# Kernel optimization log

Measured on AMD Instinct MI355X. Metric: run time of the kernel, lower is better.

Reference implementation:

```python
import jax, jax.numpy as jnp
import numpy as np

B, N, E, H = 32, 512, 256, 8
HD = E // H
EPS = 1e-5

def setup_inputs() -> dict:
    key = jax.random.key(0)
    ks = jax.random.split(key, 10)
    x = jax.random.normal(ks[0], (B, N, E), dtype=jnp.float32)
    # boolean masks: True = masked out. Keep diagonal unmasked so no row is fully masked.
    pre = jax.random.bernoulli(ks[1], 0.1, (B, H, N, N))
    eye = jnp.eye(N, dtype=bool)
    pre_mask = jnp.where(eye[None, None, :, :], False, pre)
    post_attn_mask = jax.random.bernoulli(ks[2], 0.1, (B, N))
    s = 1.0 / np.sqrt(E)
    in_proj_w = jax.random.uniform(ks[3], (3 * E, E), jnp.float32, -s, s)
    in_proj_b = jnp.zeros((3 * E,), jnp.float32)
    out_w = jax.random.uniform(ks[4], (E, E), jnp.float32, -s, s)
    out_b = jnp.zeros((E,), jnp.float32)
    gamma = jnp.ones((E,), jnp.float32)
    beta = jnp.zeros((E,), jnp.float32)
    return {"x": x, "pre_mask": pre_mask, "post_attn_mask": post_attn_mask,
            "in_proj_w": in_proj_w, "in_proj_b": in_proj_b,
            "out_w": out_w, "out_b": out_b, "gamma": gamma, "beta": beta}

def reference(x, pre_mask, post_attn_mask, in_proj_w, in_proj_b, out_w, out_b, gamma, beta):
    b, n, e = x.shape
    # fused qkv projection (matches nn.MultiheadAttention in_proj)
    qkv = x @ in_proj_w.T + in_proj_b            # [B,N,3E]
    q, k, v = jnp.split(qkv, 3, axis=-1)
    def heads(t):
        return t.reshape(b, n, H, HD).transpose(0, 2, 1, 3)  # [B,H,N,HD]
    q, k, v = heads(q), heads(k), heads(v)
    scores = jnp.einsum('bhqd,bhkd->bhqk', q * (HD ** -0.5), k)  # [B,H,N,N]
    scores = jnp.where(pre_mask, -1e9, scores)
    w = jax.nn.softmax(scores, axis=-1)                          # [B,H,N,N]
    o = jnp.einsum('bhqk,bhkd->bhqd', w, v)                      # [B,H,N,HD]
    o = o.transpose(0, 2, 1, 3).reshape(b, n, e)
    o = o @ out_w.T + out_b
    # post-attention mask: zero outputs of unavailable agents
    o = jnp.where(post_attn_mask[:, :, None], 0.0, o)
    # residual + LayerNorm
    y = x + o
    mu = y.mean(axis=-1, keepdims=True)
    var = y.var(axis=-1, keepdims=True)
    out = (y - mu) * jax.lax.rsqrt(var + EPS) * gamma + beta
    # attn_weights averaged over heads (PyTorch default average_attn_weights=True)
    attn_weights = w.mean(axis=1)                                # [B,N,N]
    return (out, attn_weights)
```

## Files before the change

### kernel.cpp

```cpp
#include <hip/hip_runtime.h>

#define BB 32
#define NN 512
#define EE 256
#define HH 8
#define HDD 32

typedef __attribute__((ext_vector_type(4))) float f32x4;
typedef __attribute__((ext_vector_type(8))) short s16x8;
typedef unsigned short ushort_t;
typedef unsigned int uint_t;

__device__ __forceinline__ ushort_t f2bf(float f) {
  union { float f; uint_t u; } v; v.f = f;
  uint_t r = v.u + 0x7fffu + ((v.u >> 16) & 1u);
  return (ushort_t)(r >> 16);
}
__device__ __forceinline__ uint_t pk2(float a, float b) {
  return (uint_t)f2bf(a) | ((uint_t)f2bf(b) << 16);
}
__device__ __forceinline__ float bf2f(ushort_t u) {
  union { uint_t u; float f; } v; v.u = ((uint_t)u) << 16;
  return v.f;
}

__global__ __launch_bounds__(256) void cvt_all(
    const float* __restrict__ x, const float* __restrict__ w1, const float* __restrict__ w2,
    ushort_t* __restrict__ xb, ushort_t* __restrict__ w1b, ushort_t* __restrict__ w2b) {
  const int NX = BB * NN * EE / 4;
  const int NW1 = 3 * EE * EE / 4;
  const int NW2 = EE * EE / 4;
  int i = blockIdx.x * 256 + threadIdx.x;
  const float* src; ushort_t* dst; int j;
  if (i < NX) { src = x; dst = xb; j = i; }
  else if (i < NX + NW1) { src = w1; dst = w1b; j = i - NX; }
  else if (i < NX + NW1 + NW2) { src = w2; dst = w2b; j = i - NX - NW1; }
  else return;
  float4 v = ((const float4*)src)[j];
  uint2 p; p.x = pk2(v.x, v.y); p.y = pk2(v.z, v.w);
  ((uint2*)dst)[j] = p;
}

__global__ __launch_bounds__(256) void qkv_mfma(
    const ushort_t* __restrict__ xb, const ushort_t* __restrict__ wb,
    const float* __restrict__ bias,
    ushort_t* __restrict__ Q, ushort_t* __restrict__ K, ushort_t* __restrict__ Vt) {
  __shared__ ushort_t sA[128][40];
  __shared__ ushort_t sB[128][40];
  int t = threadIdx.x;
  int bj = blockIdx.x % 6, bm = blockIdx.x / 6;
  int m0 = bm * 128, j0 = bj * 128;
  int w4 = t >> 6, lane = t & 63, quad = lane >> 4, l16 = lane & 15;
  int wy = w4 >> 1, wx = w4 & 1;
  f32x4 acc[4][4];
  #pragma unroll
  for (int a = 0; a < 4; a++)
    #pragma unroll
    for (int b = 0; b < 4; b++) acc[a][b] = (f32x4){0.f, 0.f, 0.f, 0.f};
  int sr2 = t >> 2, sc2 = (t & 3) * 8;
  for (int kk = 0; kk < 256; kk += 32) {
    __syncthreads();
    #pragma unroll
    for (int p = 0; p < 2; p++) {
      int r = sr2 + 64 * p;
      *(s16x8*)&sA[r][sc2] = *(const s16x8*)&xb[(size_t)(m0 + r) * 256 + kk + sc2];
      *(s16x8*)&sB[r][sc2] = *(const s16x8*)&wb[(size_t)(j0 + r) * 256 + kk + sc2];
    }
    __syncthreads();
    s16x8 af[4], bf[4];
    #pragma unroll
    for (int mt = 0; mt < 4; mt++)
      af[mt] = *(const s16x8*)&sA[wy * 64 + mt * 16 + l16][quad * 8];
    #pragma unroll
    for (int jt = 0; jt < 4; jt++)
      bf[jt] = *(const s16x8*)&sB[wx * 64 + jt * 16 + l16][quad * 8];
    #pragma unroll
    for (int mt = 0; mt < 4; mt++)
      #pragma unroll
      for (int jt = 0; jt < 4; jt++)
        acc[mt][jt] = __builtin_amdgcn_mfma_f32_16x16x32_bf16(af[mt], bf[jt], acc[mt][jt], 0, 0, 0);
  }
  #pragma unroll
  for (int jt = 0; jt < 4; jt++) {
    int j = j0 + wx * 64 + jt * 16 + l16;
    int which = j >> 8, e0 = j & 255, h = e0 >> 5, d0 = e0 & 31;
    float b = bias[j];
    #pragma unroll
    for (int mt = 0; mt < 4; mt++) {
      #pragma unroll
      for (int r = 0; r < 4; r++) {
        int m = m0 + wy * 64 + mt * 16 + quad * 4 + r;
        int bi = m >> 9, n = m & 511;
        ushort_t val = f2bf(acc[mt][jt][r] + b);
        if (which == 2) {
          Vt[((size_t)(bi * 8 + h) * 32 + d0) * 512 + n] = val;
        } else {
          ushort_t* dst = (which == 0) ? Q : K;
          dst[((size_t)(bi * 8 + h) * 512 + n) * 32 + d0] = val;
        }
      }
    }
  }
}

__global__ __launch_bounds__(256, 4) void attn_fused(
    const ushort_t* __restrict__ Q, const ushort_t* __restrict__ K,
    const ushort_t* __restrict__ Vt, const int* __restrict__ pre_mask,
    const ushort_t* __restrict__ wob, const float* __restrict__ x,
    const float* __restrict__ out_b, const int* __restrict__ post_mask,
    const float* __restrict__ gamma, const float* __restrict__ beta,
    float* __restrict__ out, float* __restrict__ attnw) {
  __shared__ ushort_t sP[4][16 * 132];
  __shared__ float sSum[2][4][16];
  __shared__ float sO[4][16 * 33];
  __shared__ ushort_t sO16[16 * 260];
  __shared__ float sRed1[16][4];
  __shared__ float sRed2[16][4];

  int t = threadIdx.x;
  int bb = blockIdx.x >> 5;
  int q0 = (blockIdx.x & 31) << 4;
  int w = t >> 6, lane = t & 63, quad = lane >> 4, l16 = lane & 15;
  int kbase = w * 128;
  const float scale = 0.17677669529663687f;
  ushort_t* mysP = &sP[w][0];

  uint_t wm[16];
  #pragma unroll
  for (int i = 0; i < 16; i++) wm[i] = 0u;

  for (int h = 0; h < 8; h++) {
    size_t base = ((size_t)(bb * 8 + h) * 512) * 32;
    const int* mbase = pre_mask + ((size_t)(bb * 8 + h) * 512 + q0) * 512;

    int mreg[32];
    #pragma unroll
    for (int t8 = 0; t8 < 8; t8++)
      #pragma unroll
      for (int i = 0; i < 4; i++)
        mreg[t8 * 4 + i] = mbase[(quad * 4 + i) * 512 + kbase + t8 * 16 + l16];

    s16x8 afrag = *(const s16x8*)&Q[base + (size_t)(q0 + l16) * 32 + quad * 8];

    float psum[4] = {0.f, 0.f, 0.f, 0.f};
    #pragma unroll
    for (int t8 = 0; t8 < 8; t8++) {
      int n0 = kbase + t8 * 16;
      s16x8 bfrag = *(const s16x8*)&K[base + (size_t)(n0 + l16) * 32 + quad * 8];
      f32x4 acc = {0.f, 0.f, 0.f, 0.f};
      acc = __builtin_amdgcn_mfma_f32_16x16x32_bf16(afrag, bfrag, acc, 0, 0, 0);
      #pragma unroll
      for (int i = 0; i < 4; i++) {
        float e = mreg[t8 * 4 + i] ? 0.f : __expf(acc[i] * scale);
        mysP[(quad * 4 + i) * 132 + t8 * 16 + l16] = f2bf(e);
        psum[i] += e;
      }
    }
    #pragma unroll
    for (int i = 0; i < 4; i++) {
      float s = psum[i];
      s += __shfl_xor(s, 1, 64);
      s += __shfl_xor(s, 2, 64);
      s += __shfl_xor(s, 4, 64);
      s += __shfl_xor(s, 8, 64);
      psum[i] = s;
    }
    if (l16 == 0) {
      #pragma unroll
      for (int i = 0; i < 4; i++) sSum[h & 1][w][quad * 4 + i] = psum[i];
    }
    __syncthreads();

    float inv[4];
    #pragma unroll
    for (int i = 0; i < 4; i++) {
      int r = quad * 4 + i;
      inv[i] = 0.125f / (sSum[h & 1][0][r] + sSum[h & 1][1][r] + sSum[h & 1][2][r] + sSum[h & 1][3][r]);
    }
    #pragma unroll
    for (int i = 0; i < 4; i++) {
      #pragma unroll
      for (int t4 = 0; t4 < 4; t4++) {
        float a0 = inv[i] * bf2f(mysP[(quad * 4 + i) * 132 + (2 * t4) * 16 + l16]);
        float a1 = inv[i] * bf2f(mysP[(quad * 4 + i) * 132 + (2 * t4 + 1) * 16 + l16]);
        uint_t cur = wm[i * 4 + t4];
        wm[i * 4 + t4] = pk2(bf2f((ushort_t)(cur & 0xffffu)) + a0,
                             bf2f((ushort_t)(cur >> 16)) + a1);
      }
    }

    f32x4 oacc[2];
    oacc[0] = (f32x4){0.f, 0.f, 0.f, 0.f};
    oacc[1] = (f32x4){0.f, 0.f, 0.f, 0.f};
    #pragma unroll
    for (int ks = 0; ks < 4; ks++) {
      s16x8 pa = *(const s16x8*)&mysP[l16 * 132 + ks * 32 + quad * 8];
      #pragma unroll
      for (int dt = 0; dt < 2; dt++) {
        s16x8 vb = *(const s16x8*)&Vt[base + (size_t)(dt * 16 + l16) * 512 + kbase + ks * 32 + quad * 8];
        oacc[dt] = __builtin_amdgcn_mfma_f32_16x16x32_bf16(pa, vb, oacc[dt], 0, 0, 0);
      }
    }
    #pragma unroll
    for (int dt = 0; dt < 2; dt++)
      #pragma unroll
      for (int i = 0; i < 4; i++)
        sO[w][(quad * 4 + i) * 33 + dt * 16 + l16] = oacc[dt][i];
    __syncthreads();

    {
      int r = t >> 4;
      int c = (t & 15) * 2;
      float s0 = sO[0][r * 33 + c] + sO[1][r * 33 + c] + sO[2][r * 33 + c] + sO[3][r * 33 + c];
      float s1 = sO[0][r * 33 + c + 1] + sO[1][r * 33 + c + 1] + sO[2][r * 33 + c + 1] + sO[3][r * 33 + c + 1];
      float invr = 1.0f / (sSum[h & 1][0][r] + sSum[h & 1][1][r] + sSum[h & 1][2][r] + sSum[h & 1][3][r]);
      *(uint_t*)&sO16[r * 260 + h * 32 + c] = pk2(s0 * invr, s1 * invr);
    }
  }

  {
    float* arow = attnw + (size_t)(bb * 512 + q0) * 512;
    #pragma unroll
    for (int i = 0; i < 4; i++) {
      #pragma unroll
      for (int t4 = 0; t4 < 4; t4++) {
        uint_t c = wm[i * 4 + t4];
        arow[(quad * 4 + i) * 512 + kbase + (2 * t4) * 16 + l16] = bf2f((ushort_t)(c & 0xffffu));
        arow[(quad * 4 + i) * 512 + kbase + (2 * t4 + 1) * 16 + l16] = bf2f((ushort_t)(c >> 16));
      }
    }
  }
  __syncthreads();

  int jr0 = w * 64;
  f32x4 pacc[4];
  #pragma unroll
  for (int jt = 0; jt < 4; jt++) pacc[jt] = (f32x4){0.f, 0.f, 0.f, 0.f};
  #pragma unroll
  for (int kc = 0; kc < 8; kc++) {
    s16x8 pa = *(const s16x8*)&sO16[l16 * 260 + kc * 32 + quad * 8];
    #pragma unroll
    for (int jt = 0; jt < 4; jt++) {
      s16x8 bf = *(const s16x8*)&wob[(size_t)(jr0 + jt * 16 + l16) * 256 + kc * 32 + quad * 8];
      pacc[jt] = __builtin_amdgcn_mfma_f32_16x16x32_bf16(pa, bf, pacc[jt], 0, 0, 0);
    }
  }

  float g4[4], bt4[4], ob4[4];
  #pragma unroll
  for (int jt = 0; jt < 4; jt++) {
    int j = jr0 + jt * 16 + l16;
    g4[jt] = gamma[j]; bt4[jt] = beta[j]; ob4[jt] = out_b[j];
  }
  float yv[4][4];
  #pragma unroll
  for (int i = 0; i < 4; i++) {
    int r = quad * 4 + i;
    int m = bb * 512 + q0 + r;
    bool msk = post_mask[m] != 0;
    float s1 = 0.f, s2 = 0.f;
    #pragma unroll
    for (int jt = 0; jt < 4; jt++) {
      int j = jr0 + jt * 16 + l16;
      float p = msk ? 0.f : (pacc[jt][i] + ob4[jt]);
      float yy = x[(size_t)m * 256 + j] + p;
      yv[i][jt] = yy; s1 += yy; s2 += yy * yy;
    }
    s1 += __shfl_xor(s1, 1, 64); s1 += __shfl_xor(s1, 2, 64);
    s1 += __shfl_xor(s1, 4, 64); s1 += __shfl_xor(s1, 8, 64);
    s2 += __shfl_xor(s2, 1, 64); s2 += __shfl_xor(s2, 2, 64);
    s2 += __shfl_xor(s2, 4, 64); s2 += __shfl_xor(s2, 8, 64);
    if (l16 == 0) { sRed1[r][w] = s1; sRed2[r][w] = s2; }
  }
  __syncthreads();
  #pragma unroll
  for (int i = 0; i < 4; i++) {
    int r = quad * 4 + i;
    int m = bb * 512 + q0 + r;
    float S1 = sRed1[r][0] + sRed1[r][1] + sRed1[r][2] + sRed1[r][3];
    float S2 = sRed2[r][0] + sRed2[r][1] + sRed2[r][2] + sRed2[r][3];
    float mu = S1 * (1.0f / 256.0f);
    float var = S2 * (1.0f / 256.0f) - mu * mu;
    float rstd = rsqrtf(var + 1e-5f);
    #pragma unroll
    for (int jt = 0; jt < 4; jt++) {
      int j = jr0 + jt * 16 + l16;
      out[(size_t)m * 256 + j] = (yv[i][jt] - mu) * rstd * g4[jt] + bt4[jt];
    }
  }
}

extern "C" void kernel_launch(void* const* d_in, const int* in_sizes, int n_in,
                              void* d_out, int out_size, void* d_ws, size_t ws_size,
                              hipStream_t stream) {
  const float* x       = (const float*)d_in[0];
  const int*   pre_m   = (const int*)d_in[1];
  const int*   post_m  = (const int*)d_in[2];
  const float* in_w    = (const float*)d_in[3];
  const float* in_b    = (const float*)d_in[4];
  const float* out_w   = (const float*)d_in[5];
  const float* out_b   = (const float*)d_in[6];
  const float* gamma   = (const float*)d_in[7];
  const float* beta    = (const float*)d_in[8];
  float* out   = (float*)d_out;
  float* attnw = out + (size_t)BB * NN * EE;
  ushort_t* Q   = (ushort_t*)d_ws;
  ushort_t* K   = Q  + (size_t)BB * HH * NN * HDD;
  ushort_t* Vt  = K  + (size_t)BB * HH * NN * HDD;
  ushort_t* xb  = Vt + (size_t)BB * HH * NN * HDD;
  ushort_t* wib = xb + (size_t)BB * NN * EE;
  ushort_t* wob = wib + (size_t)3 * EE * EE;

  const int NCVT = BB * NN * EE / 4 + 3 * EE * EE / 4 + EE * EE / 4;
  cvt_all<<<dim3((NCVT + 255) / 256), dim3(256), 0, stream>>>(x, in_w, out_w, xb, wib, wob);
  qkv_mfma<<<dim3(768), dim3(256), 0, stream>>>(xb, wib, in_b, Q, K, Vt);
  attn_fused<<<dim3(1024), dim3(256), 0, stream>>>(Q, K, Vt, pre_m, wob, x, out_b, post_m,
                                                   gamma, beta, out, attnw);
}
```

Measured before the change: 461.5 us.

## Pack the attention mask to bits alongside the QKV GEMM and read bits in attention

Extra blocks are added to the QKV projection launch. They convert the int32 pre-attention mask into a packed bitmask in workspace while the GEMM blocks run. The attention kernel then loads four uint4 bit-rows per head instead of 32 strided int32 loads, and extracts each mask bit with a shift. This aims to hide the large mask read behind the compute-bound GEMM and to cut memory latency inside the attention loop. The cost is an extra bitmask write and read in workspace, plus GEMM blocks sharing the device with bandwidth-heavy compression blocks.

```diff
diff --git a/kernel.cpp b/kernel.cpp
--- a/kernel.cpp
+++ b/kernel.cpp
@@ -41,13 +41,36 @@
   ((uint2*)dst)[j] = p;
 }
 
-__global__ __launch_bounds__(256) void qkv_mfma(
+#define NQKV 768
+#define NCMP 1280
+__global__ __launch_bounds__(256) void qkv_compress(
     const ushort_t* __restrict__ xb, const ushort_t* __restrict__ wb,
     const float* __restrict__ bias,
-    ushort_t* __restrict__ Q, ushort_t* __restrict__ K, ushort_t* __restrict__ Vt) {
+    ushort_t* __restrict__ Q, ushort_t* __restrict__ K, ushort_t* __restrict__ Vt,
+    const int* __restrict__ pre_mask, uint_t* __restrict__ mbits) {
   __shared__ ushort_t sA[128][40];
   __shared__ ushort_t sB[128][40];
   int t = threadIdx.x;
+
+  if (blockIdx.x >= NQKV) {
+    const int NWRD = BB * HH * NN * NN / 32;
+    const int STR = NCMP * 256;
+    for (int wi = (blockIdx.x - NQKV) * 256 + t; wi < NWRD; wi += STR) {
+      const int4* p = (const int4*)pre_mask + (size_t)wi * 8;
+      uint_t bits = 0u;
+      #pragma unroll
+      for (int j = 0; j < 8; j++) {
+        int4 v = p[j];
+        bits |= (uint_t)(v.x != 0) << (j * 4);
+        bits |= (uint_t)(v.y != 0) << (j * 4 + 1);
+        bits |= (uint_t)(v.z != 0) << (j * 4 + 2);
+        bits |= (uint_t)(v.w != 0) << (j * 4 + 3);
+      }
+      mbits[wi] = bits;
+    }
+    return;
+  }
+
   int bj = blockIdx.x % 6, bm = blockIdx.x / 6;
   int m0 = bm * 128, j0 = bj * 128;
   int w4 = t >> 6, lane = t & 63, quad = lane >> 4, l16 = lane & 15;
@@ -105,7 +128,7 @@
 
 __global__ __launch_bounds__(256, 4) void attn_fused(
     const ushort_t* __restrict__ Q, const ushort_t* __restrict__ K,
-    const ushort_t* __restrict__ Vt, const int* __restrict__ pre_mask,
+    const ushort_t* __restrict__ Vt, const uint_t* __restrict__ mbits32,
     const ushort_t* __restrict__ wob, const float* __restrict__ x,
     const float* __restrict__ out_b, const int* __restrict__ post_mask,
     const float* __restrict__ gamma, const float* __restrict__ beta,
@@ -131,16 +154,14 @@
 
   for (int h = 0; h < 8; h++) {
     size_t base = ((size_t)(bb * 8 + h) * 512) * 32;
-    const int* mbase = pre_mask + ((size_t)(bb * 8 + h) * 512 + q0) * 512;
-
-    int mreg[32];
-    #pragma unroll
-    for (int t8 = 0; t8 < 8; t8++)
-      #pragma unroll
-      for (int i = 0; i < 4; i++)
-        mreg[t8 * 4 + i] = mbase[(quad * 4 + i) * 512 + kbase + t8 * 16 + l16];
+    const uint_t* mb = mbits32 + ((size_t)(bb * 8 + h) * 512 + q0) * 16 + (kbase >> 5);
 
     s16x8 afrag = *(const s16x8*)&Q[base + (size_t)(q0 + l16) * 32 + quad * 8];
+
+    uint4 mrow[4];
+    #pragma unroll
+    for (int i = 0; i < 4; i++)
+      mrow[i] = *(const uint4*)&mb[(quad * 4 + i) * 16];
 
     float psum[4] = {0.f, 0.f, 0.f, 0.f};
     #pragma unroll
@@ -149,9 +170,11 @@
       s16x8 bfrag = *(const s16x8*)&K[base + (size_t)(n0 + l16) * 32 + quad * 8];
       f32x4 acc = {0.f, 0.f, 0.f, 0.f};
       acc = __builtin_amdgcn_mfma_f32_16x16x32_bf16(afrag, bfrag, acc, 0, 0, 0);
+      int sh = (t8 & 1) * 16 + l16;
       #pragma unroll
       for (int i = 0; i < 4; i++) {
-        float e = mreg[t8 * 4 + i] ? 0.f : __expf(acc[i] * scale);
+        uint_t sel = ((const uint_t*)&mrow[i])[t8 >> 1];
+        float e = ((sel >> sh) & 1u) ? 0.f : __expf(acc[i] * scale);
         mysP[(quad * 4 + i) * 132 + t8 * 16 + l16] = f2bf(e);
         psum[i] += e;
       }
@@ -310,10 +333,11 @@
   ushort_t* xb  = Vt + (size_t)BB * HH * NN * HDD;
   ushort_t* wib = xb + (size_t)BB * NN * EE;
   ushort_t* wob = wib + (size_t)3 * EE * EE;
+  uint_t* mbits = (uint_t*)(wob + (size_t)EE * EE);
 
   const int NCVT = BB * NN * EE / 4 + 3 * EE * EE / 4 + EE * EE / 4;
   cvt_all<<<dim3((NCVT + 255) / 256), dim3(256), 0, stream>>>(x, in_w, out_w, xb, wib, wob);
-  qkv_mfma<<<dim3(768), dim3(256), 0, stream>>>(xb, wib, in_b, Q, K, Vt);
-  attn_fused<<<dim3(1024), dim3(256), 0, stream>>>(Q, K, Vt, pre_m, wob, x, out_b, post_m,
+  qkv_compress<<<dim3(NQKV + NCMP), dim3(256), 0, stream>>>(xb, wib, in_b, Q, K, Vt, pre_m, mbits);
+  attn_fused<<<dim3(1024), dim3(256), 0, stream>>>(Q, K, Vt, mbits, wob, x, out_b, post_m,
                                                    gamma, beta, out, attnw);
 }
```

After: 503.8 us. +9.2%, slower.
